# Performance work log

Measured on AMD Instinct MI355X. Metric: run time of the kernel, lower is better.

Reference implementation:

```python
import jax, jax.numpy as jnp
import numpy as np

N = 33554432
MARGIN = 1.0


def setup_inputs() -> dict:
    key = jax.random.key(0)
    k1, k2 = jax.random.split(key)
    predictions = jax.random.normal(k1, (N,), dtype=jnp.float32)
    # labels in {-1, +1}
    labels = 2 * jax.random.randint(k2, (N,), 0, 2, dtype=jnp.int32) - 1
    return {"predictions": predictions, "labels": labels}


def reference(predictions, labels):
    # Original loop math:
    #   over positives: a += 1; b += 2*(margin - p_i); c += (margin - p_i)^2
    #   over negatives: loss += a*p_j^2 + b*p_j + c
    # Vectorized as masked reductions.
    dt = predictions.dtype
    pos = labels == 1
    neg = labels == -1
    z = jnp.where(pos, MARGIN - predictions, jnp.zeros((), dt))  # margin - p on positives
    a = jnp.sum(pos.astype(dt))
    b = 2.0 * jnp.sum(z)
    c = jnp.sum(z * z)
    pn = jnp.where(neg, predictions, jnp.zeros((), dt))
    n_neg = jnp.sum(neg.astype(dt))
    loss = a * jnp.sum(pn * pn) + b * jnp.sum(pn) + c * n_neg
    return loss
```

## Files before the change

### kernel.cpp

```cpp
#include <hip/hip_runtime.h>


constexpr float MARGIN = 1.0f;

#define BANK_STRIDE 32
#define BLOCK 256
#define GPT 8
#define GROUPS_PER_BLOCK (BLOCK * GPT)

__device__ __forceinline__ float wave_reduce(float v) {
    #pragma unroll
    for (int off = 32; off > 0; off >>= 1) v += __shfl_down(v, off, 64);
    return v;
}

__global__ __launch_bounds__(BLOCK, 2) void hinge2_reduce(
    const float* __restrict__ pred, const int* __restrict__ lab,
    float* __restrict__ ws, int nvec, int nbanks, int bank_stride)
{
    const float4* p4 = reinterpret_cast<const float4*>(pred);
    const int4*   l4 = reinterpret_cast<const int4*>(lab);

    float a = 0.f, sz = 0.f, sz2 = 0.f, sp = 0.f, sp2 = 0.f;

    #define ACC(px, lx) do {                         \
        float ispos = ((lx) == 1) ? 1.0f : 0.0f;     \
        float z  = ispos * (MARGIN - (px));          \
        a   += ispos;                                \
        sz  += z;                                    \
        sz2 += z * z;                                \
        float pn = ((lx) == 1) ? 0.0f : (px);        \
        sp  += pn;                                   \
        sp2 += pn * pn;                              \
    } while (0)
    #define ACC4(p, l) do {                          \
        ACC((p).x, (l).x); ACC((p).y, (l).y);        \
        ACC((p).z, (l).z); ACC((p).w, (l).w);        \
    } while (0)

    const int base = blockIdx.x * GROUPS_PER_BLOCK + threadIdx.x;

    if (base + (GPT - 1) * BLOCK < nvec) {
        float4 pv[GPT];
        int4   lv[GPT];
        #pragma unroll
        for (int k = 0; k < GPT; ++k) pv[k] = p4[base + k * BLOCK];
        #pragma unroll
        for (int k = 0; k < GPT; ++k) lv[k] = l4[base + k * BLOCK];
        #pragma unroll
        for (int k = 0; k < GPT; ++k) ACC4(pv[k], lv[k]);
    } else {
        for (int k = 0; k < GPT; ++k) {
            int i = base + k * BLOCK;
            if (i < nvec) {
                float4 p = p4[i];
                int4   l = l4[i];
                ACC4(p, l);
            }
        }
    }
    #undef ACC4
    #undef ACC

    a   = wave_reduce(a);
    sz  = wave_reduce(sz);
    sz2 = wave_reduce(sz2);
    sp  = wave_reduce(sp);
    sp2 = wave_reduce(sp2);

    __shared__ float sdata[4][5];
    int lane = threadIdx.x & 63;
    int wid  = threadIdx.x >> 6;
    if (lane == 0) {
        sdata[wid][0] = a;
        sdata[wid][1] = sz;
        sdata[wid][2] = sz2;
        sdata[wid][3] = sp;
        sdata[wid][4] = sp2;
    }
    __syncthreads();

    if (threadIdx.x == 0) {
        float t0 = 0.f, t1 = 0.f, t2 = 0.f, t3 = 0.f, t4 = 0.f;
        #pragma unroll
        for (int w = 0; w < 4; ++w) {
            t0 += sdata[w][0];
            t1 += sdata[w][1];
            t2 += sdata[w][2];
            t3 += sdata[w][3];
            t4 += sdata[w][4];
        }
        float* bank = ws + (blockIdx.x & (nbanks - 1)) * bank_stride;
        atomicAdd(&bank[0], t0);
        atomicAdd(&bank[1], t1);
        atomicAdd(&bank[2], t2);
        atomicAdd(&bank[3], t3);
        atomicAdd(&bank[4], t4);
    }
}

__global__ __launch_bounds__(256) void hinge2_final(
    const float* __restrict__ ws,
    const float* __restrict__ pred, const int* __restrict__ lab,
    float* __restrict__ out, int n, int tail_start,
    int nbanks, int bank_stride)
{
    int t = threadIdx.x;
    float a = 0.f, sz = 0.f, sz2 = 0.f, sp = 0.f, sp2 = 0.f;
    for (int b = t; b < nbanks; b += 256) {
        const float* bank = ws + b * bank_stride;
        a   += bank[0];
        sz  += bank[1];
        sz2 += bank[2];
        sp  += bank[3];
        sp2 += bank[4];
    }
    a   = wave_reduce(a);
    sz  = wave_reduce(sz);
    sz2 = wave_reduce(sz2);
    sp  = wave_reduce(sp);
    sp2 = wave_reduce(sp2);

    __shared__ float sdata[4][5];
    int lane = t & 63, wid = t >> 6;
    if (lane == 0) {
        sdata[wid][0] = a;  sdata[wid][1] = sz; sdata[wid][2] = sz2;
        sdata[wid][3] = sp; sdata[wid][4] = sp2;
    }
    __syncthreads();

    if (t == 0) {
        double A = 0, SZ = 0, SZ2 = 0, SP = 0, SP2 = 0;
        #pragma unroll
        for (int w = 0; w < 4; ++w) {
            A   += sdata[w][0];
            SZ  += sdata[w][1];
            SZ2 += sdata[w][2];
            SP  += sdata[w][3];
            SP2 += sdata[w][4];
        }
        for (int i = tail_start; i < n; ++i) {
            float p = pred[i];
            if (lab[i] == 1) {
                double z = (double)MARGIN - (double)p;
                A += 1.0; SZ += z; SZ2 += z * z;
            } else {
                SP += (double)p; SP2 += (double)p * (double)p;
            }
        }
        double loss = A * SP2 + 2.0 * SZ * SP + SZ2 * ((double)n - A);
        out[0] = (float)loss;
    }
}

extern "C" void kernel_launch(void* const* d_in, const int* in_sizes, int n_in,
                              void* d_out, int out_size, void* d_ws, size_t ws_size,
                              hipStream_t stream)
{
    const float* pred = (const float*)d_in[0];
    const int*   lab  = (const int*)d_in[1];
    float*       out  = (float*)d_out;
    float*       ws   = (float*)d_ws;

    int n    = in_sizes[0];
    int nvec = n >> 2;
    int tail = nvec << 2;

    int bank_stride = BANK_STRIDE;
    size_t max_banks = ws_size / (bank_stride * sizeof(float));
    int nbanks = 1;
    if (max_banks == 0) { bank_stride = 5; nbanks = 1; }
    else { while (nbanks * 2 <= (int)max_banks && nbanks < 256) nbanks <<= 1; }

    hipMemsetAsync(ws, 0, (size_t)nbanks * bank_stride * sizeof(float), stream);

    int blocks = (nvec + GROUPS_PER_BLOCK - 1) / GROUPS_PER_BLOCK;
    if (blocks < 1) blocks = 1;
    hinge2_reduce<<<blocks, BLOCK, 0, stream>>>(pred, lab, ws, nvec, nbanks, bank_stride);
    hinge2_final<<<1, BLOCK, 0, stream>>>(ws, pred, lab, out, n, tail, nbanks, bank_stride);
}
```

Measured before the change: 276.6 us.

## Stage input loads through LDS with global_load_lds and halve per-block work

Replaces the register-staged vector loads with direct global-to-LDS transfers (global_load_lds, 16 bytes per lane), then reads the staged data back from shared memory for accumulation. Per-thread work drops from 8 to 4 float4 groups, which doubles the block count and the number of atomic adds, and the launch-bounds occupancy hint is removed. The aim is to cut VGPR pressure and raise memory-level parallelism. The cost is 32 KB of LDS per block, which limits occupancy, plus an added LDS round trip and barrier.

After: 276.1 us. Within noise of the previous version (-0.2%).

```diff
diff --git a/kernel.cpp b/kernel.cpp
--- a/kernel.cpp
+++ b/kernel.cpp
@@ -5,8 +5,12 @@
 
 #define BANK_STRIDE 32
 #define BLOCK 256
-#define GPT 8
-#define GROUPS_PER_BLOCK (BLOCK * GPT)
+#define WAVES 4
+#define SLOTS 4
+#define GROUPS_PER_BLOCK (BLOCK * SLOTS)
+
+#define GLOBAL_AS __attribute__((address_space(1)))
+#define LDS_AS    __attribute__((address_space(3)))
 
 __device__ __forceinline__ float wave_reduce(float v) {
     #pragma unroll
@@ -14,12 +18,15 @@
     return v;
 }
 
-__global__ __launch_bounds__(BLOCK, 2) void hinge2_reduce(
+__global__ __launch_bounds__(BLOCK) void hinge2_reduce(
     const float* __restrict__ pred, const int* __restrict__ lab,
     float* __restrict__ ws, int nvec, int nbanks, int bank_stride)
 {
     const float4* p4 = reinterpret_cast<const float4*>(pred);
     const int4*   l4 = reinterpret_cast<const int4*>(lab);
+
+    __shared__ float4 sp_[WAVES][SLOTS][64];
+    __shared__ int4   sl_[WAVES][SLOTS][64];
 
     float a = 0.f, sz = 0.f, sz2 = 0.f, sp = 0.f, sp2 = 0.f;
 
@@ -38,23 +45,39 @@
         ACC((p).z, (l).z); ACC((p).w, (l).w);        \
     } while (0)
 
-    const int base = blockIdx.x * GROUPS_PER_BLOCK + threadIdx.x;
-
-    if (base + (GPT - 1) * BLOCK < nvec) {
-        float4 pv[GPT];
-        int4   lv[GPT];
-        #pragma unroll
-        for (int k = 0; k < GPT; ++k) pv[k] = p4[base + k * BLOCK];
-        #pragma unroll
-        for (int k = 0; k < GPT; ++k) lv[k] = l4[base + k * BLOCK];
-        #pragma unroll
-        for (int k = 0; k < GPT; ++k) ACC4(pv[k], lv[k]);
+    const int lane = threadIdx.x & 63;
+    const int wid  = threadIdx.x >> 6;
+    const int blockBase = blockIdx.x * GROUPS_PER_BLOCK;
+
+    if (blockBase + GROUPS_PER_BLOCK <= nvec) {
+        #pragma unroll
+        for (int s = 0; s < SLOTS; ++s) {
+            int g = blockBase + wid * (SLOTS * 64) + s * 64 + lane;
+            __builtin_amdgcn_global_load_lds(
+                (const GLOBAL_AS void*)(p4 + g),
+                (LDS_AS void*)&sp_[wid][s][0], 16, 0, 0);
+        }
+        #pragma unroll
+        for (int s = 0; s < SLOTS; ++s) {
+            int g = blockBase + wid * (SLOTS * 64) + s * 64 + lane;
+            __builtin_amdgcn_global_load_lds(
+                (const GLOBAL_AS void*)(l4 + g),
+                (LDS_AS void*)&sl_[wid][s][0], 16, 0, 0);
+        }
+        __syncthreads();
+
+        #pragma unroll
+        for (int s = 0; s < SLOTS; ++s) {
+            float4 p = sp_[wid][s][lane];
+            int4   l = sl_[wid][s][lane];
+            ACC4(p, l);
+        }
     } else {
-        for (int k = 0; k < GPT; ++k) {
-            int i = base + k * BLOCK;
-            if (i < nvec) {
-                float4 p = p4[i];
-                int4   l = l4[i];
+        for (int s = 0; s < SLOTS; ++s) {
+            int g = blockBase + wid * (SLOTS * 64) + s * 64 + lane;
+            if (g < nvec) {
+                float4 p = p4[g];
+                int4   l = l4[g];
                 ACC4(p, l);
             }
         }
@@ -68,9 +91,7 @@
     sp  = wave_reduce(sp);
     sp2 = wave_reduce(sp2);
 
-    __shared__ float sdata[4][5];
-    int lane = threadIdx.x & 63;
-    int wid  = threadIdx.x >> 6;
+    __shared__ float sdata[WAVES][5];
     if (lane == 0) {
         sdata[wid][0] = a;
         sdata[wid][1] = sz;
@@ -83,7 +104,7 @@
     if (threadIdx.x == 0) {
         float t0 = 0.f, t1 = 0.f, t2 = 0.f, t3 = 0.f, t4 = 0.f;
         #pragma unroll
-        for (int w = 0; w < 4; ++w) {
+        for (int w = 0; w < WAVES; ++w) {
             t0 += sdata[w][0];
             t1 += sdata[w][1];
             t2 += sdata[w][2];
```
